# Optimization experiments

Hardware: AMD Instinct MI355X
Metric: run time of the kernel (lower is better)

The kernel has to match this reference:

```python
import jax, jax.numpy as jnp
import numpy as np

N_HEAD = 8
N_FEAT = 512
EPS = 1e-6


def _forward(query, Wq, bq, Wk, bk, Wv, bv, Wo, bo):
    # query: (bsz, tgt_len, E). key = value = query (self-attention).
    bsz, tgt_len, E = query.shape
    head_dim = E // N_HEAD
    n = bsz * N_HEAD

    # Faithful to torch: .view((L, N, E)) is a RESHAPE, not a transpose.
    x = query.reshape(tgt_len, bsz, E)

    q = x @ Wq.T + bq
    k = x @ Wk.T + bk
    v = x @ Wv.T + bv

    # relu activation on q, k (act_fun='relu')
    q = jax.nn.relu(q).reshape(tgt_len, n, head_dim).swapaxes(0, 1)  # (n, L, d)
    k = jax.nn.relu(k).reshape(tgt_len, n, head_dim).swapaxes(0, 1)  # (n, L, d)
    v = v.reshape(tgt_len, n, head_dim).swapaxes(0, 1)               # (n, L, d)

    # cos reweighting: weight_index = pi/2 * arange(1, m+1) / m
    m = tgt_len
    idx = (np.pi / 2) * jnp.arange(1, m + 1, dtype=query.dtype) / m  # (L,)
    idx = idx[None, :, None]                                         # (1, L, 1)
    q_ = jnp.concatenate([q * jnp.sin(idx), q * jnp.cos(idx)], axis=-1)  # (n, L, 2d)
    k_ = jnp.concatenate([k * jnp.sin(idx), k * jnp.cos(idx)], axis=-1)  # (n, L, 2d)

    # causal linear attention via cumsum recurrence
    kv = jnp.einsum('nld,nlm->nldm', k_, v)          # (n, L, 2d, d)
    kv_cum = jnp.cumsum(kv, axis=1)                  # (n, L, 2d, d)
    qkv = jnp.einsum('nld,nldm->nlm', q_, kv_cum)    # (n, L, d)
    k_cum = jnp.cumsum(k_, axis=1)                   # (n, L, 2d)
    denom = jnp.clip(jnp.einsum('nld,nld->nl', q_, k_cum), EPS, None)
    attn = qkv / denom[..., None]                    # (n, L, d)

    attn = attn.swapaxes(0, 1).reshape(tgt_len, bsz, E)
    out = attn @ Wo.T + bo
    # Faithful to torch: final .view back to (bsz, tgt_len, E) is a reshape.
    return out.reshape(bsz, tgt_len, N_FEAT)


def setup_inputs() -> dict:
    key = jax.random.key(0)
    ks = jax.random.split(key, 9)
    bsz, L, E = 2, 1024, N_FEAT
    scale = 0.02
    return {
        'query': jax.random.normal(ks[0], (bsz, L, E), dtype=jnp.float32),
        'Wq': jax.random.normal(ks[1], (E, E), dtype=jnp.float32) * scale,
        'bq': jnp.zeros((E,), dtype=jnp.float32),
        'Wk': jax.random.normal(ks[2], (E, E), dtype=jnp.float32) * scale,
        'bk': jnp.zeros((E,), dtype=jnp.float32),
        'Wv': jax.random.normal(ks[3], (E, E), dtype=jnp.float32) * scale,
        'bv': jnp.zeros((E,), dtype=jnp.float32),
        'Wo': jax.random.normal(ks[4], (E, E), dtype=jnp.float32) * scale,
        'bo': jnp.zeros((E,), dtype=jnp.float32),
    }


def reference(query, Wq, bq, Wk, bk, Wv, bv, Wo, bo):
    return _forward(query, Wq, bq, Wk, bk, Wv, bv, Wo, bo)
```

## Files before the change

kernel.cpp:

```cpp
#include <hip/hip_runtime.h>
#include <math.h>

#define LSEQ 1024
#define EDIM 512
#define HD 64
#define CCH 32
#define NCH 32
#define DFEAT 128

typedef unsigned short u16;
typedef short bf16x8 __attribute__((ext_vector_type(8)));
typedef float f32x4 __attribute__((ext_vector_type(4)));

__device__ __forceinline__ u16 f2bf(float f) {
    unsigned u = __float_as_uint(f);
    unsigned r = (u + 0x7fffu + ((u >> 16) & 1u)) >> 16;
    return (u16)r;
}
__device__ __forceinline__ float bf2f(u16 x) {
    return __uint_as_float((unsigned)x << 16);
}
__device__ __forceinline__ void async16(void* lds, const void* g) {
    __builtin_amdgcn_global_load_lds(
        (const __attribute__((address_space(1))) unsigned int*)g,
        (__attribute__((address_space(3))) unsigned int*)lds, 16, 0, 0);
}

__global__ __launch_bounds__(256) void cast_kernel(
    const float* __restrict__ X,  const float* __restrict__ Wq,
    const float* __restrict__ Wk, const float* __restrict__ Wv,
    const float* __restrict__ Wo, u16* __restrict__ Xb, u16* __restrict__ Wb)
{
    int i = blockIdx.x * 256 + threadIdx.x;
    const float* src; u16* dst; int off;
    if (i < 262144)      { src = X;  dst = Xb;          off = i; }
    else if (i < 327680) { src = Wq; dst = Wb;          off = i - 262144; }
    else if (i < 393216) { src = Wk; dst = Wb + 262144; off = i - 327680; }
    else if (i < 458752) { src = Wv; dst = Wb + 524288; off = i - 393216; }
    else                 { src = Wo; dst = Wb + 786432; off = i - 458752; }
    float4 v = *(const float4*)&src[(size_t)off * 4];
    ushort4 o; o.x = f2bf(v.x); o.y = f2bf(v.y); o.z = f2bf(v.z); o.w = f2bf(v.w);
    *(ushort4*)&dst[(size_t)off * 4] = o;
}

__global__ __launch_bounds__(256) void qkv_mfma_kernel(
    const u16* __restrict__ Xb, const u16* __restrict__ Wb,
    const float* __restrict__ bq, const float* __restrict__ bk, const float* __restrict__ bv,
    u16* __restrict__ qf, u16* __restrict__ kf, u16* __restrict__ vf)
{
    const int z = blockIdx.z;
    const u16* __restrict__ W = Wb + (size_t)z * 262144;
    const float* __restrict__ bias = (z == 0) ? bq : (z == 1) ? bk : bv;
    const int r0 = blockIdx.x * 128;
    const int j0 = blockIdx.y * 128;
    __shared__ u16 As[128 * 32];
    __shared__ u16 Bs[128 * 32];
    const int t = threadIdx.x;
    const int wave = t >> 6, lane = t & 63;
    const int wm = (wave & 1) * 64, wn = (wave >> 1) * 64;
    const int cl = lane & 15, rg4 = lane >> 4;
    f32x4 acc[4][4];
    #pragma unroll
    for (int fi = 0; fi < 4; ++fi)
        #pragma unroll
        for (int fj = 0; fj < 4; ++fj) acc[fi][fj] = (f32x4){0.f, 0.f, 0.f, 0.f};

    for (int kb = 0; kb < 512; kb += 32) {
        #pragma unroll
        for (int i = 0; i < 2; ++i) {
            int chunk = i * 256 + t;
            int row = chunk >> 2, kg = chunk & 3;
            async16(&As[(size_t)(i * 256 + wave * 64) * 8], Xb + (size_t)(r0 + row) * 512 + kb + kg * 8);
            async16(&Bs[(size_t)(i * 256 + wave * 64) * 8], W  + (size_t)(j0 + row) * 512 + kb + kg * 8);
        }
        __syncthreads();
        bf16x8 af[4], bg[4];
        #pragma unroll
        for (int f = 0; f < 4; ++f) {
            af[f] = *(const bf16x8*)&As[(wm + f * 16 + cl) * 32 + rg4 * 8];
            bg[f] = *(const bf16x8*)&Bs[(wn + f * 16 + cl) * 32 + rg4 * 8];
        }
        #pragma unroll
        for (int fi = 0; fi < 4; ++fi)
            #pragma unroll
            for (int fj = 0; fj < 4; ++fj)
                acc[fi][fj] = __builtin_amdgcn_mfma_f32_16x16x32_bf16(af[fi], bg[fj], acc[fi][fj], 0, 0, 0);
        __syncthreads();
    }

    float biasv[4];
    #pragma unroll
    for (int fj = 0; fj < 4; ++fj) biasv[fj] = bias[j0 + wn + fj * 16 + cl];
    #pragma unroll
    for (int fi = 0; fi < 4; ++fi) {
        #pragma unroll
        for (int rr = 0; rr < 4; ++rr) {
            const int row_g = r0 + wm + fi * 16 + rg4 * 4 + rr;
            const int l = row_g >> 1, bb = row_g & 1;
            if (z < 2) {
                float ang = 1.5707963267948966f * (float)(l + 1) * (1.0f / 1024.0f);
                float sv, cv;
                sincosf(ang, &sv, &cv);
                u16* __restrict__ dst = (z == 0) ? qf : kf;
                #pragma unroll
                for (int fj = 0; fj < 4; ++fj) {
                    const int jg = j0 + wn + fj * 16 + cl;
                    float y = fmaxf(acc[fi][fj][rr] + biasv[fj], 0.f);
                    const int h = jg >> 6, d = jg & 63;
                    size_t base = (size_t)((bb * 8 + h) * LSEQ + l) * DFEAT;
                    dst[base + d]      = f2bf(y * sv);
                    dst[base + d + 64] = f2bf(y * cv);
                }
            } else {
                #pragma unroll
                for (int fj = 0; fj < 4; ++fj) {
                    const int jg = j0 + wn + fj * 16 + cl;
                    float y = acc[fi][fj][rr] + biasv[fj];
                    const int h = jg >> 6, d = jg & 63;
                    vf[(size_t)((bb * 8 + h) * LSEQ + l) * HD + d] = f2bf(y);
                }
            }
        }
    }
}

__global__ __launch_bounds__(256) void chunk_sum_kernel(
    const u16* __restrict__ kf, const u16* __restrict__ vf,
    float* __restrict__ KVc, float* __restrict__ K1c)
{
    const int n = blockIdx.x >> 5;
    const int c = blockIdx.x & 31;
    __shared__ u16 Ks[32 * 128];
    __shared__ u16 VT[64 * 32];
    const int t = threadIdx.x;
    const int wave = t >> 6, lane = t & 63;
    const int cl = lane & 15, rg4 = lane >> 4;
    const u16* kbase = kf + (size_t)(n * LSEQ + c * CCH) * DFEAT;
    const u16* vbase = vf + (size_t)(n * LSEQ + c * CCH) * HD;
    #pragma unroll
    for (int i = 0; i < 2; ++i)
        async16(&Ks[(size_t)(i * 256 + wave * 64) * 8], kbase + (size_t)(i * 256 + t) * 8);
    {
        u16 tmp[8];
        #pragma unroll
        for (int j = 0; j < 8; ++j) tmp[j] = vbase[(wave * 8 + j) * HD + lane];
        *(bf16x8*)&VT[lane * 32 + wave * 8] = *(bf16x8*)tmp;
    }
    __syncthreads();

    bf16x8 af = *(const bf16x8*)&VT[(wave * 16 + cl) * 32 + rg4 * 8];
    f32x4 acc[8];
    #pragma unroll
    for (int ni = 0; ni < 8; ++ni) {
        u16 bt[8];
        #pragma unroll
        for (int j = 0; j < 8; ++j)
            bt[j] = Ks[(rg4 * 8 + j) * 128 + ni * 16 + cl];
        acc[ni] = __builtin_amdgcn_mfma_f32_16x16x32_bf16(af, *(bf16x8*)bt,
                                                          (f32x4){0.f,0.f,0.f,0.f}, 0, 0, 0);
    }
    float* out = KVc + (size_t)(n * NCH + c) * (HD * DFEAT);
    #pragma unroll
    for (int ni = 0; ni < 8; ++ni)
        #pragma unroll
        for (int r = 0; r < 4; ++r) {
            int m = wave * 16 + rg4 * 4 + r;
            out[(size_t)m * 128 + ni * 16 + cl] = acc[ni][r];
        }
    if (t < 128) {
        float s = 0.f;
        #pragma unroll
        for (int l = 0; l < 32; ++l) s += bf2f(Ks[l * 128 + t]);
        K1c[(size_t)(n * NCH + c) * DFEAT + t] = s;
    }
}

__global__ __launch_bounds__(256) void prefix_kernel(
    const float* __restrict__ KVc, const float* __restrict__ K1c,
    u16* __restrict__ Spt, float* __restrict__ K1p)
{
    const int bx = blockIdx.x, t = threadIdx.x;
    if (bx < 512) {
        const int n = bx >> 5;
        const int e = (bx & 31) * 256 + t;
        const float* src = KVc + (size_t)n * NCH * 8192 + e;
        u16* dst = Spt + (size_t)n * NCH * 8192 + e;
        float v[32];
        #pragma unroll
        for (int c = 0; c < 32; ++c) v[c] = src[(size_t)c * 8192];
        float run = 0.f;
        #pragma unroll
        for (int c = 0; c < 32; ++c) { dst[(size_t)c * 8192] = f2bf(run); run += v[c]; }
    } else {
        const int idx = (bx - 512) * 256 + t;
        const int n = idx >> 7, d = idx & 127;
        const float* src = K1c + (size_t)n * NCH * DFEAT + d;
        float* dst = K1p + (size_t)n * NCH * DFEAT + d;
        float v[32];
        #pragma unroll
        for (int c = 0; c < 32; ++c) v[c] = src[c * DFEAT];
        float run = 0.f;
        #pragma unroll
        for (int c = 0; c < 32; ++c) { dst[c * DFEAT] = run; run += v[c]; }
    }
}

__global__ __launch_bounds__(256) void attn_kernel(
    const u16* __restrict__ qf, const u16* __restrict__ kf, const u16* __restrict__ vf,
    const u16* __restrict__ Spt, const float* __restrict__ K1p,
    u16* __restrict__ Amb)
{
    const int n = blockIdx.x >> 5;
    const int c = blockIdx.x & 31;
    __shared__ u16 Qs[32 * 136];
    __shared__ u16 Ks[32 * 136];
    __shared__ u16 VT[64 * 32];
    __shared__ u16 Am[32 * 32];
    __shared__ float K1s[128];
    __shared__ float dsum2[2][32];
    __shared__ float qk1[32];
    const int t = threadIdx.x;
    const int wave = t >> 6, lane = t & 63;
    const int cl = lane & 15, rg4 = lane >> 4;
    const int mi = wave >> 1, nh = wave & 1;

    const u16* qbase = qf + (size_t)(n * LSEQ + c * CCH) * DFEAT;
    const u16* kbase = kf + (size_t)(n * LSEQ + c * CCH) * DFEAT;
    const u16* vbase = vf + (size_t)(n * LSEQ + c * CCH) * HD;
    const u16* spbase = Spt + (size_t)(n * NCH + c) * 8192;

    bf16x8 spf[2][4];
    #pragma unroll
    for (int ni2 = 0; ni2 < 2; ++ni2)
        #pragma unroll
        for (int ks = 0; ks < 4; ++ks)
            spf[ni2][ks] = *(const bf16x8*)&spbase[((2 * nh + ni2) * 16 + cl) * 128 + ks * 32 + rg4 * 8];

    #pragma unroll
    for (int i = 0; i < 2; ++i) {
        int chunk = i * 256 + t;
        int row = chunk >> 4, c8 = chunk & 15;
        *(bf16x8*)&Qs[row * 136 + c8 * 8] = *(const bf16x8*)&qbase[row * 128 + c8 * 8];
        *(bf16x8*)&Ks[row * 136 + c8 * 8] = *(const bf16x8*)&kbase[row * 128 + c8 * 8];
    }
    {
        u16 tmp[8];
        #pragma unroll
        for (int j = 0; j < 8; ++j) tmp[j] = vbase[(wave * 8 + j) * HD + lane];
        *(bf16x8*)&VT[lane * 32 + wave * 8] = *(bf16x8*)tmp;
    }
    if (t < 128) K1s[t] = K1p[(size_t)(n * NCH + c) * DFEAT + t];
    __syncthreads();

    f32x4 a_acc = (f32x4){0.f, 0.f, 0.f, 0.f};
    #pragma unroll
    for (int ks = 0; ks < 4; ++ks) {
        bf16x8 aq = *(const bf16x8*)&Qs[(mi * 16 + cl) * 136 + ks * 32 + rg4 * 8];
        bf16x8 bk = *(const bf16x8*)&Ks[(nh * 16 + cl) * 136 + ks * 32 + rg4 * 8];
        a_acc = __builtin_amdgcn_mfma_f32_16x16x32_bf16(aq, bk, a_acc, 0, 0, 0);
    }
    #pragma unroll
    for (int r = 0; r < 4; ++r) {
        int l_loc = mi * 16 + rg4 * 4 + r;
        int lp_loc = nh * 16 + cl;
        float v = (lp_loc <= l_loc) ? a_acc[r] : 0.f;
        Am[l_loc * 32 + lp_loc] = f2bf(v);
        float s = v;
        s += __shfl_xor(s, 1); s += __shfl_xor(s, 2);
        s += __shfl_xor(s, 4); s += __shfl_xor(s, 8);
        if (cl == 0) dsum2[nh][l_loc] = s;
    }
    {
        int row = wave * 8 + (lane >> 3), seg = lane & 7;
        float s = 0.f;
        #pragma unroll
        for (int j = 0; j < 16; ++j) {
            int d = seg * 16 + j;
            s += bf2f(Qs[row * 136 + d]) * K1s[d];
        }
        s += __shfl_xor(s, 1); s += __shfl_xor(s, 2); s += __shfl_xor(s, 4);
        if (seg == 0) qk1[row] = s;
    }
    __syncthreads();

    f32x4 oacc[2] = {(f32x4){0.f,0.f,0.f,0.f}, (f32x4){0.f,0.f,0.f,0.f}};
    #pragma unroll
    for (int ks = 0; ks < 4; ++ks) {
        bf16x8 aq = *(const bf16x8*)&Qs[(mi * 16 + cl) * 136 + ks * 32 + rg4 * 8];
        #pragma unroll
        for (int ni2 = 0; ni2 < 2; ++ni2)
            oacc[ni2] = __builtin_amdgcn_mfma_f32_16x16x32_bf16(aq, spf[ni2][ks], oacc[ni2], 0, 0, 0);
    }
    {
        bf16x8 aa = *(const bf16x8*)&Am[(mi * 16 + cl) * 32 + rg4 * 8];
        #pragma unroll
        for (int ni2 = 0; ni2 < 2; ++ni2) {
            bf16x8 bv = *(const bf16x8*)&VT[((2 * nh + ni2) * 16 + cl) * 32 + rg4 * 8];
            oacc[ni2] = __builtin_amdgcn_mfma_f32_16x16x32_bf16(aa, bv, oacc[ni2], 0, 0, 0);
        }
    }
    const int bb = n >> 3, h = n & 7;
    #pragma unroll
    for (int r = 0; r < 4; ++r) {
        int l_loc = mi * 16 + rg4 * 4 + r;
        float den = fmaxf(dsum2[0][l_loc] + dsum2[1][l_loc] + qk1[l_loc], 1e-6f);
        float inv = 1.0f / den;
        int rrow = (c * CCH + l_loc) * 2 + bb;
        #pragma unroll
        for (int ni2 = 0; ni2 < 2; ++ni2) {
            int m = (2 * nh + ni2) * 16 + cl;
            Amb[(size_t)rrow * EDIM + h * 64 + m] = f2bf(oacc[ni2][r] * inv);
        }
    }
}

__global__ __launch_bounds__(256) void out_mfma_kernel(
    const u16* __restrict__ Amb, const u16* __restrict__ Wob,
    const float* __restrict__ bo, float* __restrict__ out)
{
    const int r0 = blockIdx.x * 128;
    const int j0 = blockIdx.y * 128;
    __shared__ u16 As[128 * 32];
    __shared__ u16 Bs[128 * 32];
    const int t = threadIdx.x;
    const int wave = t >> 6, lane = t & 63;
    const int wm = (wave & 1) * 64, wn = (wave >> 1) * 64;
    const int cl = lane & 15, rg4 = lane >> 4;
    f32x4 acc[4][4];
    #pragma unroll
    for (int fi = 0; fi < 4; ++fi)
        #pragma unroll
        for (int fj = 0; fj < 4; ++fj) acc[fi][fj] = (f32x4){0.f, 0.f, 0.f, 0.f};

    for (int kb = 0; kb < 512; kb += 32) {
        #pragma unroll
        for (int i = 0; i < 2; ++i) {
            int chunk = i * 256 + t;
            int row = chunk >> 2, kg = chunk & 3;
            async16(&As[(size_t)(i * 256 + wave * 64) * 8], Amb + (size_t)(r0 + row) * 512 + kb + kg * 8);
            async16(&Bs[(size_t)(i * 256 + wave * 64) * 8], Wob + (size_t)(j0 + row) * 512 + kb + kg * 8);
        }
        __syncthreads();
        bf16x8 af[4], bg[4];
        #pragma unroll
        for (int f = 0; f < 4; ++f) {
            af[f] = *(const bf16x8*)&As[(wm + f * 16 + cl) * 32 + rg4 * 8];
            bg[f] = *(const bf16x8*)&Bs[(wn + f * 16 + cl) * 32 + rg4 * 8];
        }
        #pragma unroll
        for (int fi = 0; fi < 4; ++fi)
            #pragma unroll
            for (int fj = 0; fj < 4; ++fj)
                acc[fi][fj] = __builtin_amdgcn_mfma_f32_16x16x32_bf16(af[fi], bg[fj], acc[fi][fj], 0, 0, 0);
        __syncthreads();
    }

    float bov[4];
    #pragma unroll
    for (int fj = 0; fj < 4; ++fj) bov[fj] = bo[j0 + wn + fj * 16 + cl];
    #pragma unroll
    for (int fi = 0; fi < 4; ++fi)
        #pragma unroll
        for (int rr = 0; rr < 4; ++rr) {
            const int row_g = r0 + wm + fi * 16 + rg4 * 4 + rr;
            #pragma unroll
            for (int fj = 0; fj < 4; ++fj)
                out[(size_t)row_g * EDIM + j0 + wn + fj * 16 + cl] = acc[fi][fj][rr] + bov[fj];
        }
}

extern "C" void kernel_launch(void* const* d_in, const int* in_sizes, int n_in,
                              void* d_out, int out_size, void* d_ws, size_t ws_size,
                              hipStream_t stream) {
    const float* X  = (const float*)d_in[0];
    const float* Wq = (const float*)d_in[1]; const float* bq = (const float*)d_in[2];
    const float* Wk = (const float*)d_in[3]; const float* bk = (const float*)d_in[4];
    const float* Wv = (const float*)d_in[5]; const float* bv = (const float*)d_in[6];
    const float* Wo = (const float*)d_in[7]; const float* bo = (const float*)d_in[8];
    float* out = (float*)d_out;
    char* base = (char*)d_ws;
    u16*   qf  = (u16*)(base + 0);
    u16*   kf  = (u16*)(base + 4194304);
    u16*   vf  = (u16*)(base + 8388608);
    float* KVc = (float*)(base + 10485760);
    float* K1c = (float*)(base + 27262976);
    u16*   Spt = (u16*)(base + 27525120);
    float* K1p = (float*)(base + 35913728);
    u16*   Amb = (u16*)(base + 36175872);
    u16*   Xb  = (u16*)(base + 38273024);
    u16*   Wb  = (u16*)(base + 40370176);

    hipLaunchKernelGGL(cast_kernel, dim3(2048), dim3(256), 0, stream,
                       X, Wq, Wk, Wv, Wo, Xb, Wb);
    hipLaunchKernelGGL(qkv_mfma_kernel, dim3(16, 4, 3), dim3(256), 0, stream,
                       Xb, Wb, bq, bk, bv, qf, kf, vf);
    hipLaunchKernelGGL(chunk_sum_kernel, dim3(512), dim3(256), 0, stream, kf, vf, KVc, K1c);
    hipLaunchKernelGGL(prefix_kernel, dim3(520), dim3(256), 0, stream, KVc, K1c, Spt, K1p);
    hipLaunchKernelGGL(attn_kernel, dim3(512), dim3(256), 0, stream,
                       qf, kf, vf, Spt, K1p, Amb);
    hipLaunchKernelGGL(out_mfma_kernel, dim3(16, 4), dim3(256), 0, stream,
                       Amb, Wb + 786432, bo, out);
}
```

Baseline: 119.4 us.

## Fuse chunk-sum, prefix and attention kernels into one cooperative grid-synced kernel

Merges the three middle kernels (per-chunk KV sums, cross-chunk prefix scan, intra-chunk attention) into one cooperative kernel launch, separated by grid.sync barriers and sharing a union of LDS buffers. It also stages V through LDS with an async load and transposes K in LDS, so the chunk-sum MFMA operands come from vector LDS reads instead of scalar gathers. The aim is to remove two kernel launch gaps and tail effects. The cost is two grid-wide barriers, and the cooperative launch requires all 512 blocks to be co-resident.

```diff
diff --git a/kernel.cpp b/kernel.cpp
--- a/kernel.cpp
+++ b/kernel.cpp
@@ -1,5 +1,8 @@
 #include <hip/hip_runtime.h>
+#include <hip/hip_cooperative_groups.h>
 #include <math.h>
+
+namespace cg = cooperative_groups;
 
 #define LSEQ 1024
 #define EDIM 512
@@ -124,192 +127,203 @@
     }
 }
 
-__global__ __launch_bounds__(256) void chunk_sum_kernel(
-    const u16* __restrict__ kf, const u16* __restrict__ vf,
-    float* __restrict__ KVc, float* __restrict__ K1c)
+__global__ __launch_bounds__(256) void mid_fused_kernel(
+    const u16* __restrict__ qf, const u16* __restrict__ kf, const u16* __restrict__ vf,
+    float* __restrict__ KVc, float* __restrict__ K1c,
+    u16* __restrict__ Spt, float* __restrict__ K1p, u16* __restrict__ Amb)
 {
-    const int n = blockIdx.x >> 5;
-    const int c = blockIdx.x & 31;
-    __shared__ u16 Ks[32 * 128];
-    __shared__ u16 VT[64 * 32];
+    cg::grid_group grid = cg::this_grid();
+    __shared__ union {
+        struct {
+            u16 Ks[32 * 128];
+            u16 KT[128 * 32];
+            u16 Vs[32 * 64];
+            u16 VT[64 * 32];
+        } p1;
+        struct {
+            u16 Qs[32 * 136];
+            u16 Ks[32 * 136];
+            u16 VT[64 * 32];
+            u16 Am[32 * 32];
+            float K1s[128];
+            float dsum2[2][32];
+            float qk1[32];
+        } p3;
+    } sh;
+    const int b = blockIdx.x;
+    const int n = b >> 5, c = b & 31;
     const int t = threadIdx.x;
     const int wave = t >> 6, lane = t & 63;
     const int cl = lane & 15, rg4 = lane >> 4;
-    const u16* kbase = kf + (size_t)(n * LSEQ + c * CCH) * DFEAT;
-    const u16* vbase = vf + (size_t)(n * LSEQ + c * CCH) * HD;
-    #pragma unroll
-    for (int i = 0; i < 2; ++i)
-        async16(&Ks[(size_t)(i * 256 + wave * 64) * 8], kbase + (size_t)(i * 256 + t) * 8);
+
     {
-        u16 tmp[8];
-        #pragma unroll
-        for (int j = 0; j < 8; ++j) tmp[j] = vbase[(wave * 8 + j) * HD + lane];
-        *(bf16x8*)&VT[lane * 32 + wave * 8] = *(bf16x8*)tmp;
-    }
-    __syncthreads();
-
-    bf16x8 af = *(const bf16x8*)&VT[(wave * 16 + cl) * 32 + rg4 * 8];
-    f32x4 acc[8];
-    #pragma unroll
-    for (int ni = 0; ni < 8; ++ni) {
-        u16 bt[8];
-        #pragma unroll
-        for (int j = 0; j < 8; ++j)
-            bt[j] = Ks[(rg4 * 8 + j) * 128 + ni * 16 + cl];
-        acc[ni] = __builtin_amdgcn_mfma_f32_16x16x32_bf16(af, *(bf16x8*)bt,
-                                                          (f32x4){0.f,0.f,0.f,0.f}, 0, 0, 0);
-    }
-    float* out = KVc + (size_t)(n * NCH + c) * (HD * DFEAT);
-    #pragma unroll
-    for (int ni = 0; ni < 8; ++ni)
-        #pragma unroll
-        for (int r = 0; r < 4; ++r) {
-            int m = wave * 16 + rg4 * 4 + r;
-            out[(size_t)m * 128 + ni * 16 + cl] = acc[ni][r];
-        }
-    if (t < 128) {
-        float s = 0.f;
-        #pragma unroll
-        for (int l = 0; l < 32; ++l) s += bf2f(Ks[l * 128 + t]);
-        K1c[(size_t)(n * NCH + c) * DFEAT + t] = s;
-    }
-}
-
-__global__ __launch_bounds__(256) void prefix_kernel(
-    const float* __restrict__ KVc, const float* __restrict__ K1c,
-    u16* __restrict__ Spt, float* __restrict__ K1p)
-{
-    const int bx = blockIdx.x, t = threadIdx.x;
-    if (bx < 512) {
-        const int n = bx >> 5;
-        const int e = (bx & 31) * 256 + t;
+        const u16* kbase = kf + (size_t)(n * LSEQ + c * CCH) * DFEAT;
+        const u16* vbase = vf + (size_t)(n * LSEQ + c * CCH) * HD;
+        #pragma unroll
+        for (int i = 0; i < 2; ++i)
+            async16(&sh.p1.Ks[(i * 256 + wave * 64) * 8], kbase + (size_t)(i * 256 + t) * 8);
+        async16(&sh.p1.Vs[(wave * 64) * 8], vbase + (size_t)t * 8);
+        __syncthreads();
+        {
+            int m = t & 63, l0 = (t >> 6) * 8;
+            u16 tmp[8];
+            #pragma unroll
+            for (int j = 0; j < 8; ++j) tmp[j] = sh.p1.Vs[(l0 + j) * 64 + m];
+            *(bf16x8*)&sh.p1.VT[m * 32 + l0] = *(bf16x8*)tmp;
+        }
+        {
+            int d = t & 127, l0 = (t >> 7) * 16;
+            #pragma unroll
+            for (int half = 0; half < 2; ++half) {
+                u16 tmp[8];
+                #pragma unroll
+                for (int j = 0; j < 8; ++j) tmp[j] = sh.p1.Ks[(l0 + half * 8 + j) * 128 + d];
+                *(bf16x8*)&sh.p1.KT[d * 32 + l0 + half * 8] = *(bf16x8*)tmp;
+            }
+        }
+        __syncthreads();
+        bf16x8 af = *(const bf16x8*)&sh.p1.VT[(wave * 16 + cl) * 32 + rg4 * 8];
+        f32x4 acc[8];
+        #pragma unroll
+        for (int ni = 0; ni < 8; ++ni) {
+            bf16x8 bfr = *(const bf16x8*)&sh.p1.KT[(ni * 16 + cl) * 32 + rg4 * 8];
+            acc[ni] = __builtin_amdgcn_mfma_f32_16x16x32_bf16(af, bfr, (f32x4){0.f,0.f,0.f,0.f}, 0, 0, 0);
+        }
+        float* outp = KVc + (size_t)(n * NCH + c) * (HD * DFEAT);
+        #pragma unroll
+        for (int ni = 0; ni < 8; ++ni)
+            #pragma unroll
+            for (int r = 0; r < 4; ++r)
+                outp[(size_t)(wave * 16 + rg4 * 4 + r) * 128 + ni * 16 + cl] = acc[ni][r];
+        if (t < 128) {
+            float s = 0.f;
+            #pragma unroll
+            for (int g = 0; g < 4; ++g) {
+                bf16x8 kv = *(const bf16x8*)&sh.p1.KT[t * 32 + g * 8];
+                #pragma unroll
+                for (int j = 0; j < 8; ++j) s += bf2f(((u16*)&kv)[j]);
+            }
+            K1c[(size_t)(n * NCH + c) * DFEAT + t] = s;
+        }
+    }
+    __threadfence();
+    grid.sync();
+
+    {
+        const int e = c * 256 + t;
         const float* src = KVc + (size_t)n * NCH * 8192 + e;
         u16* dst = Spt + (size_t)n * NCH * 8192 + e;
         float v[32];
         #pragma unroll
-        for (int c = 0; c < 32; ++c) v[c] = src[(size_t)c * 8192];
+        for (int cc = 0; cc < 32; ++cc) v[cc] = src[(size_t)cc * 8192];
         float run = 0.f;
         #pragma unroll
-        for (int c = 0; c < 32; ++c) { dst[(size_t)c * 8192] = f2bf(run); run += v[c]; }
-    } else {
-        const int idx = (bx - 512) * 256 + t;
-        const int n = idx >> 7, d = idx & 127;
-        const float* src = K1c + (size_t)n * NCH * DFEAT + d;
-        float* dst = K1p + (size_t)n * NCH * DFEAT + d;
-        float v[32];
-        #pragma unroll
-        for (int c = 0; c < 32; ++c) v[c] = src[c * DFEAT];
-        float run = 0.f;
-        #pragma unroll
-        for (int c = 0; c < 32; ++c) { dst[c * DFEAT] = run; run += v[c]; }
-    }
-}
-
-__global__ __launch_bounds__(256) void attn_kernel(
-    const u16* __restrict__ qf, const u16* __restrict__ kf, const u16* __restrict__ vf,
-    const u16* __restrict__ Spt, const float* __restrict__ K1p,
-    u16* __restrict__ Amb)
-{
-    const int n = blockIdx.x >> 5;
-    const int c = blockIdx.x & 31;
-    __shared__ u16 Qs[32 * 136];
-    __shared__ u16 Ks[32 * 136];
-    __shared__ u16 VT[64 * 32];
-    __shared__ u16 Am[32 * 32];
-    __shared__ float K1s[128];
-    __shared__ float dsum2[2][32];
-    __shared__ float qk1[32];
-    const int t = threadIdx.x;
-    const int wave = t >> 6, lane = t & 63;
-    const int cl = lane & 15, rg4 = lane >> 4;
-    const int mi = wave >> 1, nh = wave & 1;
-
-    const u16* qbase = qf + (size_t)(n * LSEQ + c * CCH) * DFEAT;
-    const u16* kbase = kf + (size_t)(n * LSEQ + c * CCH) * DFEAT;
-    const u16* vbase = vf + (size_t)(n * LSEQ + c * CCH) * HD;
-    const u16* spbase = Spt + (size_t)(n * NCH + c) * 8192;
-
-    bf16x8 spf[2][4];
-    #pragma unroll
-    for (int ni2 = 0; ni2 < 2; ++ni2)
-        #pragma unroll
-        for (int ks = 0; ks < 4; ++ks)
-            spf[ni2][ks] = *(const bf16x8*)&spbase[((2 * nh + ni2) * 16 + cl) * 128 + ks * 32 + rg4 * 8];
-
-    #pragma unroll
-    for (int i = 0; i < 2; ++i) {
-        int chunk = i * 256 + t;
-        int row = chunk >> 4, c8 = chunk & 15;
-        *(bf16x8*)&Qs[row * 136 + c8 * 8] = *(const bf16x8*)&qbase[row * 128 + c8 * 8];
-        *(bf16x8*)&Ks[row * 136 + c8 * 8] = *(const bf16x8*)&kbase[row * 128 + c8 * 8];
-    }
+        for (int cc = 0; cc < 32; ++cc) { dst[(size_t)cc * 8192] = f2bf(run); run += v[cc]; }
+        if (b < 8) {
+            const int idx = b * 256 + t;
+            const int nn = idx >> 7, d = idx & 127;
+            const float* s2 = K1c + (size_t)nn * NCH * DFEAT + d;
+            float* d2 = K1p + (size_t)nn * NCH * DFEAT + d;
+            float v2[32];
+            #pragma unroll
+            for (int cc = 0; cc < 32; ++cc) v2[cc] = s2[cc * DFEAT];
+            float run2 = 0.f;
+            #pragma unroll
+            for (int cc = 0; cc < 32; ++cc) { d2[cc * DFEAT] = run2; run2 += v2[cc]; }
+        }
+    }
+    __threadfence();
+    grid.sync();
+
     {
-        u16 tmp[8];
-        #pragma unroll
-        for (int j = 0; j < 8; ++j) tmp[j] = vbase[(wave * 8 + j) * HD + lane];
-        *(bf16x8*)&VT[lane * 32 + wave * 8] = *(bf16x8*)tmp;
-    }
-    if (t < 128) K1s[t] = K1p[(size_t)(n * NCH + c) * DFEAT + t];
-    __syncthreads();
-
-    f32x4 a_acc = (f32x4){0.f, 0.f, 0.f, 0.f};
-    #pragma unroll
-    for (int ks = 0; ks < 4; ++ks) {
-        bf16x8 aq = *(const bf16x8*)&Qs[(mi * 16 + cl) * 136 + ks * 32 + rg4 * 8];
-        bf16x8 bk = *(const bf16x8*)&Ks[(nh * 16 + cl) * 136 + ks * 32 + rg4 * 8];
-        a_acc = __builtin_amdgcn_mfma_f32_16x16x32_bf16(aq, bk, a_acc, 0, 0, 0);
-    }
-    #pragma unroll
-    for (int r = 0; r < 4; ++r) {
-        int l_loc = mi * 16 + rg4 * 4 + r;
-        int lp_loc = nh * 16 + cl;
-        float v = (lp_loc <= l_loc) ? a_acc[r] : 0.f;
-        Am[l_loc * 32 + lp_loc] = f2bf(v);
-        float s = v;
-        s += __shfl_xor(s, 1); s += __shfl_xor(s, 2);
-        s += __shfl_xor(s, 4); s += __shfl_xor(s, 8);
-        if (cl == 0) dsum2[nh][l_loc] = s;
-    }
-    {
-        int row = wave * 8 + (lane >> 3), seg = lane & 7;
-        float s = 0.f;
-        #pragma unroll
-        for (int j = 0; j < 16; ++j) {
-            int d = seg * 16 + j;
-            s += bf2f(Qs[row * 136 + d]) * K1s[d];
-        }
-        s += __shfl_xor(s, 1); s += __shfl_xor(s, 2); s += __shfl_xor(s, 4);
-        if (seg == 0) qk1[row] = s;
-    }
-    __syncthreads();
-
-    f32x4 oacc[2] = {(f32x4){0.f,0.f,0.f,0.f}, (f32x4){0.f,0.f,0.f,0.f}};
-    #pragma unroll
-    for (int ks = 0; ks < 4; ++ks) {
-        bf16x8 aq = *(const bf16x8*)&Qs[(mi * 16 + cl) * 136 + ks * 32 + rg4 * 8];
+        const int mi = wave >> 1, nh = wave & 1;
+        const u16* qbase = qf + (size_t)(n * LSEQ + c * CCH) * DFEAT;
+        const u16* kbase = kf + (size_t)(n * LSEQ + c * CCH) * DFEAT;
+        const u16* vbase = vf + (size_t)(n * LSEQ + c * CCH) * HD;
+        const u16* spbase = Spt + (size_t)(n * NCH + c) * 8192;
+
+        bf16x8 spf[2][4];
         #pragma unroll
         for (int ni2 = 0; ni2 < 2; ++ni2)
-            oacc[ni2] = __builtin_amdgcn_mfma_f32_16x16x32_bf16(aq, spf[ni2][ks], oacc[ni2], 0, 0, 0);
-    }
-    {
-        bf16x8 aa = *(const bf16x8*)&Am[(mi * 16 + cl) * 32 + rg4 * 8];
-        #pragma unroll
-        for (int ni2 = 0; ni2 < 2; ++ni2) {
-            bf16x8 bv = *(const bf16x8*)&VT[((2 * nh + ni2) * 16 + cl) * 32 + rg4 * 8];
-            oacc[ni2] = __builtin_amdgcn_mfma_f32_16x16x32_bf16(aa, bv, oacc[ni2], 0, 0, 0);
-        }
-    }
-    const int bb = n >> 3, h = n & 7;
-    #pragma unroll
-    for (int r = 0; r < 4; ++r) {
-        int l_loc = mi * 16 + rg4 * 4 + r;
-        float den = fmaxf(dsum2[0][l_loc] + dsum2[1][l_loc] + qk1[l_loc], 1e-6f);
-        float inv = 1.0f / den;
-        int rrow = (c * CCH + l_loc) * 2 + bb;
-        #pragma unroll
-        for (int ni2 = 0; ni2 < 2; ++ni2) {
-            int m = (2 * nh + ni2) * 16 + cl;
-            Amb[(size_t)rrow * EDIM + h * 64 + m] = f2bf(oacc[ni2][r] * inv);
+            #pragma unroll
+            for (int ks = 0; ks < 4; ++ks)
+                spf[ni2][ks] = *(const bf16x8*)&spbase[((2 * nh + ni2) * 16 + cl) * 128 + ks * 32 + rg4 * 8];
+
+        #pragma unroll
+        for (int i = 0; i < 2; ++i) {
+            int chunk = i * 256 + t;
+            int row = chunk >> 4, c8 = chunk & 15;
+            *(bf16x8*)&sh.p3.Qs[row * 136 + c8 * 8] = *(const bf16x8*)&qbase[row * 128 + c8 * 8];
+            *(bf16x8*)&sh.p3.Ks[row * 136 + c8 * 8] = *(const bf16x8*)&kbase[row * 128 + c8 * 8];
+        }
+        {
+            u16 tmp[8];
+            #pragma unroll
+            for (int j = 0; j < 8; ++j) tmp[j] = vbase[(wave * 8 + j) * HD + lane];
+            *(bf16x8*)&sh.p3.VT[lane * 32 + wave * 8] = *(bf16x8*)tmp;
+        }
+        if (t < 128) sh.p3.K1s[t] = K1p[(size_t)(n * NCH + c) * DFEAT + t];
+        __syncthreads();
+
+        f32x4 a_acc = (f32x4){0.f, 0.f, 0.f, 0.f};
+        #pragma unroll
+        for (int ks = 0; ks < 4; ++ks) {
+            bf16x8 aq = *(const bf16x8*)&sh.p3.Qs[(mi * 16 + cl) * 136 + ks * 32 + rg4 * 8];
+            bf16x8 bk = *(const bf16x8*)&sh.p3.Ks[(nh * 16 + cl) * 136 + ks * 32 + rg4 * 8];
+            a_acc = __builtin_amdgcn_mfma_f32_16x16x32_bf16(aq, bk, a_acc, 0, 0, 0);
+        }
+        #pragma unroll
+        for (int r = 0; r < 4; ++r) {
+            int l_loc = mi * 16 + rg4 * 4 + r;
+            int lp_loc = nh * 16 + cl;
+            float v = (lp_loc <= l_loc) ? a_acc[r] : 0.f;
+            sh.p3.Am[l_loc * 32 + lp_loc] = f2bf(v);
+            float s = v;
+            s += __shfl_xor(s, 1); s += __shfl_xor(s, 2);
+            s += __shfl_xor(s, 4); s += __shfl_xor(s, 8);
+            if (cl == 0) sh.p3.dsum2[nh][l_loc] = s;
+        }
+        {
+            int row = wave * 8 + (lane >> 3), seg = lane & 7;
+            float s = 0.f;
+            #pragma unroll
+            for (int j = 0; j < 16; ++j) {
+                int d = seg * 16 + j;
+                s += bf2f(sh.p3.Qs[row * 136 + d]) * sh.p3.K1s[d];
+            }
+            s += __shfl_xor(s, 1); s += __shfl_xor(s, 2); s += __shfl_xor(s, 4);
+            if (seg == 0) sh.p3.qk1[row] = s;
+        }
+        __syncthreads();
+
+        f32x4 oacc[2] = {(f32x4){0.f,0.f,0.f,0.f}, (f32x4){0.f,0.f,0.f,0.f}};
+        #pragma unroll
+        for (int ks = 0; ks < 4; ++ks) {
+            bf16x8 aq = *(const bf16x8*)&sh.p3.Qs[(mi * 16 + cl) * 136 + ks * 32 + rg4 * 8];
+            #pragma unroll
+            for (int ni2 = 0; ni2 < 2; ++ni2)
+                oacc[ni2] = __builtin_amdgcn_mfma_f32_16x16x32_bf16(aq, spf[ni2][ks], oacc[ni2], 0, 0, 0);
+        }
+        {
+            bf16x8 aa = *(const bf16x8*)&sh.p3.Am[(mi * 16 + cl) * 32 + rg4 * 8];
+            #pragma unroll
+            for (int ni2 = 0; ni2 < 2; ++ni2) {
+                bf16x8 bv = *(const bf16x8*)&sh.p3.VT[((2 * nh + ni2) * 16 + cl) * 32 + rg4 * 8];
+                oacc[ni2] = __builtin_amdgcn_mfma_f32_16x16x32_bf16(aa, bv, oacc[ni2], 0, 0, 0);
+            }
+        }
+        const int bb = n >> 3, h = n & 7;
+        #pragma unroll
+        for (int r = 0; r < 4; ++r) {
+            int l_loc = mi * 16 + rg4 * 4 + r;
+            float den = fmaxf(sh.p3.dsum2[0][l_loc] + sh.p3.dsum2[1][l_loc] + sh.p3.qk1[l_loc], 1e-6f);
+            float inv = 1.0f / den;
+            int rrow = (c * CCH + l_loc) * 2 + bb;
+            #pragma unroll
+            for (int ni2 = 0; ni2 < 2; ++ni2) {
+                int m = (2 * nh + ni2) * 16 + cl;
+                Amb[(size_t)rrow * EDIM + h * 64 + m] = f2bf(oacc[ni2][r] * inv);
+            }
         }
     }
 }
@@ -394,10 +408,13 @@
                        X, Wq, Wk, Wv, Wo, Xb, Wb);
     hipLaunchKernelGGL(qkv_mfma_kernel, dim3(16, 4, 3), dim3(256), 0, stream,
                        Xb, Wb, bq, bk, bv, qf, kf, vf);
-    hipLaunchKernelGGL(chunk_sum_kernel, dim3(512), dim3(256), 0, stream, kf, vf, KVc, K1c);
-    hipLaunchKernelGGL(prefix_kernel, dim3(520), dim3(256), 0, stream, KVc, K1c, Spt, K1p);
-    hipLaunchKernelGGL(attn_kernel, dim3(512), dim3(256), 0, stream,
-                       qf, kf, vf, Spt, K1p, Amb);
+    {
+        const u16* qf_c = qf; const u16* kf_c = kf; const u16* vf_c = vf;
+        void* kargs[] = { (void*)&qf_c, (void*)&kf_c, (void*)&vf_c,
+                          (void*)&KVc, (void*)&K1c, (void*)&Spt, (void*)&K1p, (void*)&Amb };
+        hipLaunchCooperativeKernel((void*)mid_fused_kernel, dim3(512), dim3(256),
+                                   kargs, 0, stream);
+    }
     hipLaunchKernelGGL(out_mfma_kernel, dim3(16, 4), dim3(256), 0, stream,
                        Amb, Wb + 786432, bo, out);
 }
```

Result: slower. 369.0 us (+209.0%).
